# Kernel optimization log

Measured on AMD Instinct MI355X. Metric: run time of the kernel, lower is better.

## Reference

```python
import jax, jax.numpy as jnp
import numpy as np

LN_EPS = 1e-5   # torch LayerNorm default
EPS = 1e-8      # slot-attention renorm eps
ITERS = 3


def _ln(x, g, b):
    m = jnp.mean(x, axis=-1, keepdims=True)
    v = jnp.mean(jnp.square(x - m), axis=-1, keepdims=True)
    return (x - m) * jax.lax.rsqrt(v + LN_EPS) * g + b


def _gru(x, h, W_ih, W_hh, b_ih, b_hh):
    # torch GRUCell: gates ordered r, z, n; weight_* has shape [3h, in]
    gi = x @ W_ih.T + b_ih
    gh = h @ W_hh.T + b_hh
    ir, iz, inn = jnp.split(gi, 3, axis=-1)
    hr, hz, hn = jnp.split(gh, 3, axis=-1)
    r = jax.nn.sigmoid(ir + hr)
    z = jax.nn.sigmoid(iz + hz)
    n = jnp.tanh(inn + r * hn)
    return (1.0 - z) * n + z * h


def setup_inputs() -> dict:
    key = jax.random.key(0)
    ks = jax.random.split(key, 16)
    b, n, d, n_s = 32, 4096, 256, 8
    h = max(d, 128)  # hidden_dim = max(dim, hidden_dim)
    s = 1.0 / np.sqrt(d)
    inp = {
        "inputs": jax.random.normal(ks[0], (b, n, d), jnp.float32),
        "noise": jax.random.normal(ks[1], (b, n_s, d), jnp.float32),
        "slots_mu": jax.random.normal(ks[2], (1, 1, d), jnp.float32),
        "slots_logsigma": jax.random.normal(ks[3], (1, 1, d), jnp.float32) * 0.1,
        "Wq": jax.random.uniform(ks[4], (d, d), jnp.float32, -s, s),
        "bq": jnp.zeros((d,), jnp.float32),
        "Wk": jax.random.uniform(ks[5], (d, d), jnp.float32, -s, s),
        "bk": jnp.zeros((d,), jnp.float32),
        "Wv": jax.random.uniform(ks[6], (d, d), jnp.float32, -s, s),
        "bv": jnp.zeros((d,), jnp.float32),
        "W_ih": jax.random.uniform(ks[7], (3 * d, d), jnp.float32, -s, s),
        "W_hh": jax.random.uniform(ks[8], (3 * d, d), jnp.float32, -s, s),
        "b_ih": jnp.zeros((3 * d,), jnp.float32),
        "b_hh": jnp.zeros((3 * d,), jnp.float32),
        "W1": jax.random.uniform(ks[9], (h, d), jnp.float32, -s, s),
        "b1": jnp.zeros((h,), jnp.float32),
        "W2": jax.random.uniform(ks[10], (d, h), jnp.float32, -s, s),
        "b2": jnp.zeros((d,), jnp.float32),
        "g_in": jnp.ones((d,), jnp.float32), "be_in": jnp.zeros((d,), jnp.float32),
        "g_sl": jnp.ones((d,), jnp.float32), "be_sl": jnp.zeros((d,), jnp.float32),
        "g_ff": jnp.ones((d,), jnp.float32), "be_ff": jnp.zeros((d,), jnp.float32),
    }
    return inp


def reference(inputs, noise, slots_mu, slots_logsigma, Wq, bq, Wk, bk, Wv, bv,
              W_ih, W_hh, b_ih, b_hh, W1, b1, W2, b2,
              g_in, be_in, g_sl, be_sl, g_ff, be_ff):
    b, n, d = inputs.shape
    scale = d ** (-0.5)
    # reparameterized slot init
    slots = slots_mu + jnp.exp(slots_logsigma) * noise          # [b, n_s, d]
    x = _ln(inputs, g_in, be_in)
    k = x @ Wk.T + bk                                           # [b, n, d]
    v = x @ Wv.T + bv
    attn = None
    for _ in range(ITERS):
        slots_prev = slots
        q = _ln(slots, g_sl, be_sl) @ Wq.T + bq                 # [b, n_s, d]
        dots = jnp.einsum('bid,bjd->bij', q, k) * scale         # [b, n_s, n]
        attn = jax.nn.softmax(dots, axis=1)                     # softmax over SLOTS
        attn_ = attn + EPS
        attn_ = attn_ / jnp.sum(attn_, axis=-1, keepdims=True)  # renorm over inputs
        updates = jnp.einsum('bjd,bij->bid', v, attn_)          # [b, n_s, d]
        slots = _gru(updates.reshape(-1, d), slots_prev.reshape(-1, d),
                     W_ih, W_hh, b_ih, b_hh).reshape(b, -1, d)
        pre = _ln(slots, g_ff, be_ff)
        slots = slots + (jax.nn.relu(pre @ W1.T + b1) @ W2.T + b2)
    return (slots, attn)
```

## Files before the change

kernel.cpp:

```cpp
#include <hip/hip_runtime.h>
#include <hip/hip_fp16.h>
#include <cstdint>
#include <cstddef>


#define NTOK 4096
#define DDIM 256
#define NSLOT 8
#define NBATCH 32
#define NCHK 64
#define SROWS (NBATCH * NSLOT)
#define SCALE 0.0625f
#define LN_EPS_C 1e-5f
#define ATTN_EPS_C 1e-8f

__device__ __forceinline__ void wave_reduce2(float& s, float& ss) {
#pragma unroll
  for (int off = 32; off > 0; off >>= 1) {
    s  += __shfl_down(s, off, 64);
    ss += __shfl_down(ss, off, 64);
  }
}
__device__ __forceinline__ void wave_reduce3(float& a, float& b, float& c) {
#pragma unroll
  for (int off = 32; off > 0; off >>= 1) {
    a += __shfl_down(a, off, 64);
    b += __shfl_down(b, off, 64);
    c += __shfl_down(c, off, 64);
  }
}

__global__ __launch_bounds__(256) void transpose_all_k(
    const float* __restrict__ Wq, const float* __restrict__ Wv,
    const float* __restrict__ Wih, const float* __restrict__ Whh,
    const float* __restrict__ W1, const float* __restrict__ W2,
    float* __restrict__ WqT, float* __restrict__ WvT,
    float* __restrict__ WihT, float* __restrict__ WhhT,
    float* __restrict__ W1T, float* __restrict__ W2T) {
  __shared__ float tile[32][33];
  int bz = blockIdx.x;
  const float* in; float* out; int O, bo;
  if (bz < 8)       { in = Wq;  out = WqT;  O = 256; bo = bz; }
  else if (bz < 16) { in = Wv;  out = WvT;  O = 256; bo = bz - 8; }
  else if (bz < 40) { in = Wih; out = WihT; O = 768; bo = bz - 16; }
  else if (bz < 64) { in = Whh; out = WhhT; O = 768; bo = bz - 40; }
  else if (bz < 72) { in = W1;  out = W1T;  O = 256; bo = bz - 64; }
  else              { in = W2;  out = W2T;  O = 256; bo = bz - 72; }
  int tx = threadIdx.x & 31, ty = threadIdx.x >> 5;
  int ro = bo * 32, cd = blockIdx.y * 32;
#pragma unroll
  for (int p = 0; p < 32; p += 8)
    tile[ty + p][tx] = in[(size_t)(ro + ty + p) * DDIM + cd + tx];
  __syncthreads();
#pragma unroll
  for (int p = 0; p < 32; p += 8)
    out[(size_t)(cd + ty + p) * O + ro + tx] = tile[tx][ty + p];
}

__device__ __forceinline__ void qk_tail(
    float newslot, int r, int t, const float* __restrict__ g_sl,
    const float* __restrict__ be_sl, const float* __restrict__ WqT,
    const float* __restrict__ bq, const float* __restrict__ Wk,
    const float* __restrict__ bk, const float* __restrict__ g_in,
    const float* __restrict__ be_in, float* __restrict__ qk,
    float* __restrict__ C0, float* __restrict__ G, float* ln, float* sq,
    float* red) {
  float s = newslot, ss = newslot * newslot;
  wave_reduce2(s, ss);
  int lane = t & 63, wid = t >> 6;
  if (lane == 0) { red[wid] = s; red[4 + wid] = ss; }
  __syncthreads();
  s = red[0] + red[1] + red[2] + red[3];
  ss = red[4] + red[5] + red[6] + red[7];
  float m = s * (1.f / DDIM);
  float rs = rsqrtf(ss * (1.f / DDIM) - m * m + LN_EPS_C);
  ln[t] = (newslot - m) * rs * g_sl[t] + be_sl[t];
  __syncthreads();
  float q = bq[t];
  {
    const float* p = WqT + t;
#pragma unroll 8
    for (int d = 0; d < DDIM; ++d) q = fmaf(ln[d], p[(size_t)d * DDIM], q);
  }
  sq[t] = q;
  __syncthreads();
  float a2 = 0.f;
  {
    const float* p = Wk + t;
#pragma unroll 8
    for (int o = 0; o < DDIM; ++o) a2 = fmaf(sq[o], p[(size_t)o * DDIM], a2);
  }
  float qkv = SCALE * a2;
  qk[(size_t)r * DDIM + t] = qkv;
  float v0 = q * bk[t], v1 = g_in[t] * qkv, v2 = be_in[t] * qkv;
  wave_reduce3(v0, v1, v2);
  __syncthreads();
  if (lane == 0) { red[wid] = v0; red[4 + wid] = v1; red[8 + wid] = v2; }
  __syncthreads();
  if (t == 0) {
    float qkb = SCALE * (red[0] + red[1] + red[2] + red[3]);
    float Gv = red[4] + red[5] + red[6] + red[7];
    float Bv = red[8] + red[9] + red[10] + red[11];
    C0[r] = qkb + Bv;
    G[r] = Gv;
  }
}

__global__ __launch_bounds__(256) void init_q_qk_k(
    const float* __restrict__ noise, const float* __restrict__ mu,
    const float* __restrict__ logsig, float* __restrict__ slots,
    const float* __restrict__ g_sl, const float* __restrict__ be_sl,
    const float* __restrict__ WqT, const float* __restrict__ bq,
    const float* __restrict__ Wk, const float* __restrict__ bk,
    const float* __restrict__ g_in, const float* __restrict__ be_in,
    float* __restrict__ qk, float* __restrict__ C0, float* __restrict__ G) {
  __shared__ float ln[DDIM], sq[DDIM], red[12];
  int r = blockIdx.x, t = threadIdx.x;
  float ns = mu[t] + expf(logsig[t]) * noise[(size_t)r * DDIM + t];
  slots[(size_t)r * DDIM + t] = ns;
  qk_tail(ns, r, t, g_sl, be_sl, WqT, bq, Wk, bk, g_in, be_in, qk, C0, G, ln,
          sq, red);
}

__global__ __launch_bounds__(256) void fused_attn_k(
    const float* __restrict__ X, const float* __restrict__ g,
    const float* __restrict__ be, const float* __restrict__ qk,
    const float* __restrict__ C0, const float* __restrict__ Gv,
    float* __restrict__ attn_out, float* __restrict__ S_part,
    __half* __restrict__ u_part, int write_attn) {
  __shared__ float sx[32][260];
  __shared__ float sqkg[NSLOT][DDIM];
  __shared__ float part[8][10][32];
  __shared__ float sm[32], srd[32];
  __shared__ float sC0[NSLOT], sG[NSLOT], sS[NSLOT];
  int b = blockIdx.x, c = blockIdx.y, t = threadIdx.x;
  int tj = t & 31, qd = t >> 5;
#pragma unroll
  for (int i = 0; i < NSLOT; ++i)
    sqkg[i][t] = qk[((size_t)b * NSLOT + i) * DDIM + t] * g[t];
  if (t < NSLOT) { sC0[t] = C0[b * NSLOT + t]; sG[t] = Gv[b * NSLOT + t]; sS[t] = 0.f; }
  float gt = g[t], bet = be[t];
  float acc[NSLOT] = {};
  const size_t base = (size_t)b * NTOK + (size_t)c * 64;
#pragma unroll
  for (int half = 0; half < 2; ++half) {
    __syncthreads();
#pragma unroll
    for (int it = 0; it < 8; ++it) {
      int e = it * 256 + t;
      int row = e >> 6, c4 = e & 63;
      float4 v = *(const float4*)(X + (base + half * 32 + row) * DDIM + c4 * 4);
      *(float4*)&sx[row][c4 * 4] = v;
    }
    __syncthreads();
    float s = 0.f, ss = 0.f, p[NSLOT] = {};
#pragma unroll
    for (int d4 = 0; d4 < 8; ++d4) {
      float4 xv = *(const float4*)&sx[tj][qd * 32 + d4 * 4];
      s += xv.x + xv.y + xv.z + xv.w;
      ss += xv.x * xv.x + xv.y * xv.y + xv.z * xv.z + xv.w * xv.w;
#pragma unroll
      for (int i = 0; i < NSLOT; ++i) {
        float4 qv = *(const float4*)&sqkg[i][qd * 32 + d4 * 4];
        p[i] += xv.x * qv.x + xv.y * qv.y + xv.z * qv.z + xv.w * qv.w;
      }
    }
#pragma unroll
    for (int i = 0; i < NSLOT; ++i) part[qd][i][tj] = p[i];
    part[qd][8][tj] = s;
    part[qd][9][tj] = ss;
    __syncthreads();
    if (t < 32) {
      float s1 = 0.f, s2 = 0.f;
#pragma unroll
      for (int q2 = 0; q2 < 8; ++q2) { s1 += part[q2][8][t]; s2 += part[q2][9][t]; }
      float m = s1 * (1.f / DDIM);
      float rs = rsqrtf(s2 * (1.f / DDIM) - m * m + LN_EPS_C);
      sm[t] = m;
      srd[t] = rs;
      float dots[NSLOT], mx = -1e30f;
#pragma unroll
      for (int i = 0; i < NSLOT; ++i) {
        float P1 = 0.f;
#pragma unroll
        for (int q2 = 0; q2 < 8; ++q2) P1 += part[q2][i][t];
        dots[i] = rs * (P1 - m * sG[i]) + sC0[i];
        mx = fmaxf(mx, dots[i]);
      }
      float sum = 0.f;
#pragma unroll
      for (int i = 0; i < NSLOT; ++i) { dots[i] = expf(dots[i] - mx); sum += dots[i]; }
      float inv = 1.f / sum;
#pragma unroll
      for (int i = 0; i < NSLOT; ++i) {
        float a = dots[i] * inv;
        if (write_attn)
          attn_out[((size_t)b * NSLOT + i) * NTOK + c * 64 + half * 32 + t] = a;
        float ae = a + ATTN_EPS_C;
        part[i][8][t] = ae;
        float ps = ae;
#pragma unroll
        for (int off = 16; off > 0; off >>= 1) ps += __shfl_down(ps, off, 64);
        if (t == 0) sS[i] += ps;
      }
    }
    __syncthreads();
#pragma unroll 8
    for (int jj = 0; jj < 32; ++jj) {
      float x = sx[jj][t];
      float xl = (x - sm[jj]) * srd[jj] * gt + bet;
#pragma unroll
      for (int i = 0; i < NSLOT; ++i) acc[i] = fmaf(xl, part[i][8][jj], acc[i]);
    }
  }
  __half* upb = u_part + (((size_t)b * NCHK + c) * NSLOT) * DDIM + t;
#pragma unroll
  for (int i = 0; i < NSLOT; ++i) upb[(size_t)i * DDIM] = __float2half(acc[i]);
  if (t < NSLOT) S_part[((size_t)b * NCHK + c) * NSLOT + t] = sS[t];
}

__global__ __launch_bounds__(1024) void slot_update_k(
    const __half* __restrict__ u_part, const float* __restrict__ S_part,
    const float* __restrict__ slots_in, const float* __restrict__ WvT,
    const float* __restrict__ bv, const float* __restrict__ WihT,
    const float* __restrict__ WhhT, const float* __restrict__ b_ih,
    const float* __restrict__ b_hh, const float* __restrict__ g_ff,
    const float* __restrict__ be_ff, const float* __restrict__ W1T,
    const float* __restrict__ b1, const float* __restrict__ W2T,
    const float* __restrict__ b2, const float* __restrict__ g_sl,
    const float* __restrict__ be_sl, const float* __restrict__ WqT,
    const float* __restrict__ bq, const float* __restrict__ Wk,
    const float* __restrict__ bk, const float* __restrict__ g_in,
    const float* __restrict__ be_in, float* __restrict__ slots_out,
    float* __restrict__ qk, float* __restrict__ C0, float* __restrict__ G,
    int compute_qk) {
  __shared__ float red[4][6][DDIM];
  __shared__ float su[DDIM], sh[DDIM], supd[DDIM], v1[DDIM], v2[DDIM];
  __shared__ float scal[16];
  int r = blockIdx.x, t = threadIdx.x;
  int b = r >> 3, i = r & 7;
  int o = t & 255, ks = t >> 8;
  int lane = t & 63, wid = t >> 6;
  {
    float up = 0.f;
    const __half* upp =
        u_part + (((size_t)b * NCHK + ks * 16) * NSLOT + i) * DDIM + o;
#pragma unroll
    for (int cc = 0; cc < 16; ++cc)
      up += __half2float(upp[(size_t)cc * (NSLOT * DDIM)]);
    red[ks][0][o] = up;
  }
  if (t < 64) {
    float sp = S_part[((size_t)b * NCHK + t) * NSLOT + i];
#pragma unroll
    for (int off = 32; off > 0; off >>= 1) sp += __shfl_down(sp, off, 64);
    if (t == 0) scal[0] = sp;
  }
  if (ks == 0) sh[o] = slots_in[(size_t)r * DDIM + o];
  __syncthreads();
  if (ks == 0) {
    float invS = 1.f / scal[0];
    su[o] = (red[0][0][o] + red[1][0][o] + red[2][0][o] + red[3][0][o]) * invS;
  }
  __syncthreads();
  {
    float p = 0.f;
    const float* wp = WvT + (size_t)(ks * 64) * DDIM + o;
#pragma unroll 8
    for (int dd = 0; dd < 64; ++dd)
      p = fmaf(su[ks * 64 + dd], wp[(size_t)dd * DDIM], p);
    red[ks][0][o] = p;
  }
  __syncthreads();
  if (ks == 0)
    supd[o] = bv[o] + red[0][0][o] + red[1][0][o] + red[2][0][o] + red[3][0][o];
  __syncthreads();
  {
    float p0 = 0, p1 = 0, p2 = 0, p3 = 0, p4 = 0, p5 = 0;
    const float* pi = WihT + (size_t)(ks * 64) * (3 * DDIM) + o;
    const float* ph = WhhT + (size_t)(ks * 64) * (3 * DDIM) + o;
#pragma unroll 4
    for (int dd = 0; dd < 64; ++dd) {
      float ud = supd[ks * 64 + dd], hd = sh[ks * 64 + dd];
      size_t off = (size_t)dd * (3 * DDIM);
      p0 = fmaf(ud, pi[off], p0);
      p1 = fmaf(ud, pi[off + DDIM], p1);
      p2 = fmaf(ud, pi[off + 2 * DDIM], p2);
      p3 = fmaf(hd, ph[off], p3);
      p4 = fmaf(hd, ph[off + DDIM], p4);
      p5 = fmaf(hd, ph[off + 2 * DDIM], p5);
    }
    red[ks][0][o] = p0; red[ks][1][o] = p1; red[ks][2][o] = p2;
    red[ks][3][o] = p3; red[ks][4][o] = p4; red[ks][5][o] = p5;
  }
  __syncthreads();
  if (ks == 0) {
    float air = b_ih[o] + red[0][0][o] + red[1][0][o] + red[2][0][o] + red[3][0][o];
    float aiz = b_ih[DDIM + o] + red[0][1][o] + red[1][1][o] + red[2][1][o] + red[3][1][o];
    float ain = b_ih[2 * DDIM + o] + red[0][2][o] + red[1][2][o] + red[2][2][o] + red[3][2][o];
    float ahr = b_hh[o] + red[0][3][o] + red[1][3][o] + red[2][3][o] + red[3][3][o];
    float ahz = b_hh[DDIM + o] + red[0][4][o] + red[1][4][o] + red[2][4][o] + red[3][4][o];
    float ahn = b_hh[2 * DDIM + o] + red[0][5][o] + red[1][5][o] + red[2][5][o] + red[3][5][o];
    float rg = 1.f / (1.f + expf(-(air + ahr)));
    float zg = 1.f / (1.f + expf(-(aiz + ahz)));
    float ng = tanhf(ain + rg * ahn);
    float nh = (1.f - zg) * ng + zg * sh[o];
    v1[o] = nh;
    float s2 = nh, ss2 = nh * nh;
    wave_reduce2(s2, ss2);
    if (lane == 0) { scal[wid] = s2; scal[4 + wid] = ss2; }
  }
  __syncthreads();
  if (ks == 0) {
    float sS = scal[0] + scal[1] + scal[2] + scal[3];
    float sQ = scal[4] + scal[5] + scal[6] + scal[7];
    float m = sS * (1.f / DDIM);
    float rs = rsqrtf(sQ * (1.f / DDIM) - m * m + LN_EPS_C);
    v2[o] = (v1[o] - m) * rs * g_ff[o] + be_ff[o];
  }
  __syncthreads();
  {
    float p = 0.f;
    const float* wp = W1T + (size_t)(ks * 64) * DDIM + o;
#pragma unroll 8
    for (int dd = 0; dd < 64; ++dd)
      p = fmaf(v2[ks * 64 + dd], wp[(size_t)dd * DDIM], p);
    red[ks][0][o] = p;
  }
  __syncthreads();
  if (ks == 0)
    su[o] = fmaxf(b1[o] + red[0][0][o] + red[1][0][o] + red[2][0][o] + red[3][0][o], 0.f);
  __syncthreads();
  {
    float p = 0.f;
    const float* wp = W2T + (size_t)(ks * 64) * DDIM + o;
#pragma unroll 8
    for (int dd = 0; dd < 64; ++dd)
      p = fmaf(su[ks * 64 + dd], wp[(size_t)dd * DDIM], p);
    red[ks][0][o] = p;
  }
  __syncthreads();
  if (ks == 0) {
    float out = v1[o] + b2[o] + red[0][0][o] + red[1][0][o] + red[2][0][o] + red[3][0][o];
    slots_out[(size_t)r * DDIM + o] = out;
    v2[o] = out;
  }
  __syncthreads();
  if (!compute_qk) return;
  if (ks == 0) {
    float x = v2[o];
    float s2 = x, ss2 = x * x;
    wave_reduce2(s2, ss2);
    if (lane == 0) { scal[wid] = s2; scal[4 + wid] = ss2; }
  }
  __syncthreads();
  if (ks == 0) {
    float sS = scal[0] + scal[1] + scal[2] + scal[3];
    float sQ = scal[4] + scal[5] + scal[6] + scal[7];
    float m = sS * (1.f / DDIM);
    float rs = rsqrtf(sQ * (1.f / DDIM) - m * m + LN_EPS_C);
    su[o] = (v2[o] - m) * rs * g_sl[o] + be_sl[o];
  }
  __syncthreads();
  {
    float p = 0.f;
    const float* wp = WqT + (size_t)(ks * 64) * DDIM + o;
#pragma unroll 8
    for (int dd = 0; dd < 64; ++dd)
      p = fmaf(su[ks * 64 + dd], wp[(size_t)dd * DDIM], p);
    red[ks][0][o] = p;
  }
  __syncthreads();
  if (ks == 0)
    sh[o] = bq[o] + red[0][0][o] + red[1][0][o] + red[2][0][o] + red[3][0][o];
  __syncthreads();
  {
    float p = 0.f;
    const float* wp = Wk + (size_t)(ks * 64) * DDIM + o;
#pragma unroll 8
    for (int dd = 0; dd < 64; ++dd)
      p = fmaf(sh[ks * 64 + dd], wp[(size_t)dd * DDIM], p);
    red[ks][0][o] = p;
  }
  __syncthreads();
  if (ks == 0) {
    float qkv = SCALE * (red[0][0][o] + red[1][0][o] + red[2][0][o] + red[3][0][o]);
    qk[(size_t)r * DDIM + o] = qkv;
    float v0 = sh[o] * bk[o], vG = g_in[o] * qkv, vB = be_in[o] * qkv;
    wave_reduce3(v0, vG, vB);
    if (lane == 0) { scal[wid] = v0; scal[4 + wid] = vG; scal[8 + wid] = vB; }
  }
  __syncthreads();
  if (t == 0) {
    float qkb = SCALE * (scal[0] + scal[1] + scal[2] + scal[3]);
    G[r] = scal[4] + scal[5] + scal[6] + scal[7];
    C0[r] = qkb + scal[8] + scal[9] + scal[10] + scal[11];
  }
}

extern "C" void kernel_launch(void* const* d_in, const int* in_sizes, int n_in,
                              void* d_out, int out_size, void* d_ws,
                              size_t ws_size, hipStream_t stream) {
  const float* inputs   = (const float*)d_in[0];
  const float* noise    = (const float*)d_in[1];
  const float* slots_mu = (const float*)d_in[2];
  const float* slots_ls = (const float*)d_in[3];
  const float* Wq   = (const float*)d_in[4];
  const float* bq   = (const float*)d_in[5];
  const float* Wk   = (const float*)d_in[6];
  const float* bk   = (const float*)d_in[7];
  const float* Wv   = (const float*)d_in[8];
  const float* bv   = (const float*)d_in[9];
  const float* W_ih = (const float*)d_in[10];
  const float* W_hh = (const float*)d_in[11];
  const float* b_ih = (const float*)d_in[12];
  const float* b_hh = (const float*)d_in[13];
  const float* W1   = (const float*)d_in[14];
  const float* b1   = (const float*)d_in[15];
  const float* W2   = (const float*)d_in[16];
  const float* b2   = (const float*)d_in[17];
  const float* g_in = (const float*)d_in[18];
  const float* be_in= (const float*)d_in[19];
  const float* g_sl = (const float*)d_in[20];
  const float* be_sl= (const float*)d_in[21];
  const float* g_ff = (const float*)d_in[22];
  const float* be_ff= (const float*)d_in[23];

  float* out_slots = (float*)d_out;
  float* out_attn  = (float*)d_out + SROWS * DDIM;

  float* w = (float*)d_ws;
  float* slots = w;  w += SROWS * DDIM;
  float* qk = w;     w += SROWS * DDIM;
  float* C0 = w;     w += SROWS;
  float* G = w;      w += SROWS;
  float* WqT = w;    w += DDIM * DDIM;
  float* WvT = w;    w += DDIM * DDIM;
  float* WihT = w;   w += DDIM * 3 * DDIM;
  float* WhhT = w;   w += DDIM * 3 * DDIM;
  float* W1T = w;    w += DDIM * DDIM;
  float* W2T = w;    w += DDIM * DDIM;
  float* S_part = w; w += NBATCH * NCHK * NSLOT;
  __half* u_part = (__half*)w;

  transpose_all_k<<<dim3(80, 8), 256, 0, stream>>>(
      Wq, Wv, W_ih, W_hh, W1, W2, WqT, WvT, WihT, WhhT, W1T, W2T);
  init_q_qk_k<<<SROWS, 256, 0, stream>>>(noise, slots_mu, slots_ls, slots,
                                         g_sl, be_sl, WqT, bq, Wk, bk, g_in,
                                         be_in, qk, C0, G);
  for (int it = 0; it < 3; ++it) {
    fused_attn_k<<<dim3(NBATCH, NCHK), 256, 0, stream>>>(
        inputs, g_in, be_in, qk, C0, G, out_attn, S_part, u_part,
        (it == 2) ? 1 : 0);
    float* sout = (it == 2) ? out_slots : slots;
    slot_update_k<<<SROWS, 1024, 0, stream>>>(
        u_part, S_part, slots, WvT, bv, WihT, WhhT, b_ih, b_hh, g_ff, be_ff,
        W1T, b1, W2T, b2, g_sl, be_sl, WqT, bq, Wk, bk, g_in, be_in, sout, qk,
        C0, G, (it == 2) ? 0 : 1);
  }
}
```

Baseline: 284.2 us.

## Cache LayerNormed inputs as fp16 and store weights in half precision

The first attention pass normalizes the fp32 inputs and writes them as an fp16 buffer. Later iterations read that buffer with a simpler fp16 attention kernel that no longer recomputes LayerNorm statistics. All transposed weight matrices, plus Wk, are converted to fp16 to halve weight traffic in the slot update, and the slot-init/q kernel is folded into slot_update_k. This cuts repeated fp32 reads of the large input tensor at the cost of an extra 64MB write and reduced precision.

```diff
diff --git a/kernel.cpp b/kernel.cpp
--- a/kernel.cpp
+++ b/kernel.cpp
@@ -30,23 +30,32 @@
   }
 }
 
-__global__ __launch_bounds__(256) void transpose_all_k(
+__global__ __launch_bounds__(256) void convert_weights_k(
     const float* __restrict__ Wq, const float* __restrict__ Wv,
     const float* __restrict__ Wih, const float* __restrict__ Whh,
     const float* __restrict__ W1, const float* __restrict__ W2,
-    float* __restrict__ WqT, float* __restrict__ WvT,
-    float* __restrict__ WihT, float* __restrict__ WhhT,
-    float* __restrict__ W1T, float* __restrict__ W2T) {
+    const float* __restrict__ Wk, __half* __restrict__ WqT,
+    __half* __restrict__ WvT, __half* __restrict__ WihT,
+    __half* __restrict__ WhhT, __half* __restrict__ W1T,
+    __half* __restrict__ W2T, __half* __restrict__ Wk_h) {
   __shared__ float tile[32][33];
   int bz = blockIdx.x;
-  const float* in; float* out; int O, bo;
+  int tx = threadIdx.x & 31, ty = threadIdx.x >> 5;
+  if (bz >= 80) {
+    int ro = (bz - 80) * 32, cd = blockIdx.y * 32;
+#pragma unroll
+    for (int p = 0; p < 32; p += 8)
+      Wk_h[(size_t)(ro + ty + p) * DDIM + cd + tx] =
+          __float2half(Wk[(size_t)(ro + ty + p) * DDIM + cd + tx]);
+    return;
+  }
+  const float* in; __half* out; int O, bo;
   if (bz < 8)       { in = Wq;  out = WqT;  O = 256; bo = bz; }
   else if (bz < 16) { in = Wv;  out = WvT;  O = 256; bo = bz - 8; }
   else if (bz < 40) { in = Wih; out = WihT; O = 768; bo = bz - 16; }
   else if (bz < 64) { in = Whh; out = WhhT; O = 768; bo = bz - 40; }
   else if (bz < 72) { in = W1;  out = W1T;  O = 256; bo = bz - 64; }
   else              { in = W2;  out = W2T;  O = 256; bo = bz - 72; }
-  int tx = threadIdx.x & 31, ty = threadIdx.x >> 5;
   int ro = bo * 32, cd = blockIdx.y * 32;
 #pragma unroll
   for (int p = 0; p < 32; p += 8)
@@ -54,80 +63,15 @@
   __syncthreads();
 #pragma unroll
   for (int p = 0; p < 32; p += 8)
-    out[(size_t)(cd + ty + p) * O + ro + tx] = tile[tx][ty + p];
-}
-
-__device__ __forceinline__ void qk_tail(
-    float newslot, int r, int t, const float* __restrict__ g_sl,
-    const float* __restrict__ be_sl, const float* __restrict__ WqT,
-    const float* __restrict__ bq, const float* __restrict__ Wk,
-    const float* __restrict__ bk, const float* __restrict__ g_in,
-    const float* __restrict__ be_in, float* __restrict__ qk,
-    float* __restrict__ C0, float* __restrict__ G, float* ln, float* sq,
-    float* red) {
-  float s = newslot, ss = newslot * newslot;
-  wave_reduce2(s, ss);
-  int lane = t & 63, wid = t >> 6;
-  if (lane == 0) { red[wid] = s; red[4 + wid] = ss; }
-  __syncthreads();
-  s = red[0] + red[1] + red[2] + red[3];
-  ss = red[4] + red[5] + red[6] + red[7];
-  float m = s * (1.f / DDIM);
-  float rs = rsqrtf(ss * (1.f / DDIM) - m * m + LN_EPS_C);
-  ln[t] = (newslot - m) * rs * g_sl[t] + be_sl[t];
-  __syncthreads();
-  float q = bq[t];
-  {
-    const float* p = WqT + t;
-#pragma unroll 8
-    for (int d = 0; d < DDIM; ++d) q = fmaf(ln[d], p[(size_t)d * DDIM], q);
-  }
-  sq[t] = q;
-  __syncthreads();
-  float a2 = 0.f;
-  {
-    const float* p = Wk + t;
-#pragma unroll 8
-    for (int o = 0; o < DDIM; ++o) a2 = fmaf(sq[o], p[(size_t)o * DDIM], a2);
-  }
-  float qkv = SCALE * a2;
-  qk[(size_t)r * DDIM + t] = qkv;
-  float v0 = q * bk[t], v1 = g_in[t] * qkv, v2 = be_in[t] * qkv;
-  wave_reduce3(v0, v1, v2);
-  __syncthreads();
-  if (lane == 0) { red[wid] = v0; red[4 + wid] = v1; red[8 + wid] = v2; }
-  __syncthreads();
-  if (t == 0) {
-    float qkb = SCALE * (red[0] + red[1] + red[2] + red[3]);
-    float Gv = red[4] + red[5] + red[6] + red[7];
-    float Bv = red[8] + red[9] + red[10] + red[11];
-    C0[r] = qkb + Bv;
-    G[r] = Gv;
-  }
-}
-
-__global__ __launch_bounds__(256) void init_q_qk_k(
-    const float* __restrict__ noise, const float* __restrict__ mu,
-    const float* __restrict__ logsig, float* __restrict__ slots,
-    const float* __restrict__ g_sl, const float* __restrict__ be_sl,
-    const float* __restrict__ WqT, const float* __restrict__ bq,
-    const float* __restrict__ Wk, const float* __restrict__ bk,
-    const float* __restrict__ g_in, const float* __restrict__ be_in,
-    float* __restrict__ qk, float* __restrict__ C0, float* __restrict__ G) {
-  __shared__ float ln[DDIM], sq[DDIM], red[12];
-  int r = blockIdx.x, t = threadIdx.x;
-  float ns = mu[t] + expf(logsig[t]) * noise[(size_t)r * DDIM + t];
-  slots[(size_t)r * DDIM + t] = ns;
-  qk_tail(ns, r, t, g_sl, be_sl, WqT, bq, Wk, bk, g_in, be_in, qk, C0, G, ln,
-          sq, red);
-}
-
-__global__ __launch_bounds__(256) void fused_attn_k(
+    out[(size_t)(cd + ty + p) * O + ro + tx] = __float2half(tile[tx][ty + p]);
+}
+
+__global__ __launch_bounds__(256) void fused_attn_f32_k(
     const float* __restrict__ X, const float* __restrict__ g,
     const float* __restrict__ be, const float* __restrict__ qk,
     const float* __restrict__ C0, const float* __restrict__ Gv,
-    float* __restrict__ attn_out, float* __restrict__ S_part,
-    __half* __restrict__ u_part, int write_attn) {
+    float* __restrict__ S_part, __half* __restrict__ u_part,
+    __half* __restrict__ xh_out) {
   __shared__ float sx[32][260];
   __shared__ float sqkg[NSLOT][DDIM];
   __shared__ float part[8][10][32];
@@ -193,10 +137,7 @@
       float inv = 1.f / sum;
 #pragma unroll
       for (int i = 0; i < NSLOT; ++i) {
-        float a = dots[i] * inv;
-        if (write_attn)
-          attn_out[((size_t)b * NSLOT + i) * NTOK + c * 64 + half * 32 + t] = a;
-        float ae = a + ATTN_EPS_C;
+        float ae = dots[i] * inv + ATTN_EPS_C;
         part[i][8][t] = ae;
         float ps = ae;
 #pragma unroll
@@ -209,6 +150,7 @@
     for (int jj = 0; jj < 32; ++jj) {
       float x = sx[jj][t];
       float xl = (x - sm[jj]) * srd[jj] * gt + bet;
+      xh_out[(base + half * 32 + jj) * DDIM + t] = __float2half(xl);
 #pragma unroll
       for (int i = 0; i < NSLOT; ++i) acc[i] = fmaf(xl, part[i][8][jj], acc[i]);
     }
@@ -219,21 +161,111 @@
   if (t < NSLOT) S_part[((size_t)b * NCHK + c) * NSLOT + t] = sS[t];
 }
 
+__global__ __launch_bounds__(256) void fused_attn_f16_k(
+    const __half* __restrict__ xh, const float* __restrict__ qk,
+    const float* __restrict__ qkb, float* __restrict__ attn_out,
+    float* __restrict__ S_part, __half* __restrict__ u_part, int write_attn) {
+  __shared__ __half sx[64][258];
+  __shared__ float2 sqkf[NSLOT][128];
+  __shared__ float part[4][NSLOT][64];
+  __shared__ float sa[NSLOT][64];
+  __shared__ float sC0[NSLOT], sS[NSLOT];
+  int b = blockIdx.x, c = blockIdx.y, t = threadIdx.x;
+  {
+    int i = t >> 5, p2 = t & 31;
+    const float* qr = qk + ((size_t)b * NSLOT + i) * DDIM;
+#pragma unroll
+    for (int kk = 0; kk < 4; ++kk) {
+      int col = p2 * 4 + kk;
+      sqkf[i][col] = make_float2(qr[col * 2], qr[col * 2 + 1]);
+    }
+  }
+  if (t < NSLOT) sC0[t] = qkb[b * NSLOT + t];
+  const size_t base = (size_t)b * NTOK + (size_t)c * 64;
+#pragma unroll
+  for (int it = 0; it < 8; ++it) {
+    int e = it * 256 + t;
+    int row = e >> 5, c8 = e & 31;
+    const __half* src = xh + (base + row) * DDIM + c8 * 8;
+    uint4 v = *(const uint4*)src;
+    __half2* dst = (__half2*)&sx[row][c8 * 8];
+    dst[0] = ((const __half2*)&v)[0];
+    dst[1] = ((const __half2*)&v)[1];
+    dst[2] = ((const __half2*)&v)[2];
+    dst[3] = ((const __half2*)&v)[3];
+  }
+  __syncthreads();
+  int tj = t & 63, qd = t >> 6;
+  float p[NSLOT] = {};
+  const __half2* xrow = (const __half2*)&sx[tj][qd * 64];
+#pragma unroll
+  for (int dd2 = 0; dd2 < 32; ++dd2) {
+    float2 xf = __half22float2(xrow[dd2]);
+#pragma unroll
+    for (int i = 0; i < NSLOT; ++i) {
+      float2 qf = sqkf[i][qd * 32 + dd2];
+      p[i] = fmaf(xf.x, qf.x, fmaf(xf.y, qf.y, p[i]));
+    }
+  }
+#pragma unroll
+  for (int i = 0; i < NSLOT; ++i) part[qd][i][tj] = p[i];
+  __syncthreads();
+  if (t < 64) {
+    float dots[NSLOT], mx = -1e30f;
+#pragma unroll
+    for (int i = 0; i < NSLOT; ++i) {
+      dots[i] = part[0][i][t] + part[1][i][t] + part[2][i][t] + part[3][i][t] +
+                sC0[i];
+      mx = fmaxf(mx, dots[i]);
+    }
+    float sum = 0.f;
+#pragma unroll
+    for (int i = 0; i < NSLOT; ++i) { dots[i] = expf(dots[i] - mx); sum += dots[i]; }
+    float inv = 1.f / sum;
+#pragma unroll
+    for (int i = 0; i < NSLOT; ++i) {
+      float a = dots[i] * inv;
+      if (write_attn)
+        attn_out[((size_t)b * NSLOT + i) * NTOK + c * 64 + t] = a;
+      float ae = a + ATTN_EPS_C;
+      sa[i][t] = ae;
+      float ps = ae;
+#pragma unroll
+      for (int off = 32; off > 0; off >>= 1) ps += __shfl_down(ps, off, 64);
+      if (t == 0) sS[i] = ps;
+    }
+  }
+  __syncthreads();
+  float acc[NSLOT] = {};
+#pragma unroll 8
+  for (int jj = 0; jj < 64; ++jj) {
+    float x = __half2float(sx[jj][t]);
+#pragma unroll
+    for (int i = 0; i < NSLOT; ++i) acc[i] = fmaf(x, sa[i][jj], acc[i]);
+  }
+  __half* upb = u_part + (((size_t)b * NCHK + c) * NSLOT) * DDIM + t;
+#pragma unroll
+  for (int i = 0; i < NSLOT; ++i) upb[(size_t)i * DDIM] = __float2half(acc[i]);
+  if (t < NSLOT) S_part[((size_t)b * NCHK + c) * NSLOT + t] = sS[t];
+}
+
 __global__ __launch_bounds__(1024) void slot_update_k(
     const __half* __restrict__ u_part, const float* __restrict__ S_part,
-    const float* __restrict__ slots_in, const float* __restrict__ WvT,
-    const float* __restrict__ bv, const float* __restrict__ WihT,
-    const float* __restrict__ WhhT, const float* __restrict__ b_ih,
+    const float* __restrict__ slots_in, const __half* __restrict__ WvT,
+    const float* __restrict__ bv, const __half* __restrict__ WihT,
+    const __half* __restrict__ WhhT, const float* __restrict__ b_ih,
     const float* __restrict__ b_hh, const float* __restrict__ g_ff,
-    const float* __restrict__ be_ff, const float* __restrict__ W1T,
-    const float* __restrict__ b1, const float* __restrict__ W2T,
+    const float* __restrict__ be_ff, const __half* __restrict__ W1T,
+    const float* __restrict__ b1, const __half* __restrict__ W2T,
     const float* __restrict__ b2, const float* __restrict__ g_sl,
-    const float* __restrict__ be_sl, const float* __restrict__ WqT,
-    const float* __restrict__ bq, const float* __restrict__ Wk,
+    const float* __restrict__ be_sl, const __half* __restrict__ WqT,
+    const float* __restrict__ bq, const __half* __restrict__ Wk_h,
     const float* __restrict__ bk, const float* __restrict__ g_in,
-    const float* __restrict__ be_in, float* __restrict__ slots_out,
-    float* __restrict__ qk, float* __restrict__ C0, float* __restrict__ G,
-    int compute_qk) {
+    const float* __restrict__ be_in, const float* __restrict__ noise,
+    const float* __restrict__ mu, const float* __restrict__ logsig,
+    float* __restrict__ slots_out, float* __restrict__ qk,
+    float* __restrict__ C0, float* __restrict__ qkb_out,
+    float* __restrict__ G, int init, int compute_qk) {
   __shared__ float red[4][6][DDIM];
   __shared__ float su[DDIM], sh[DDIM], supd[DDIM], v1[DDIM], v2[DDIM];
   __shared__ float scal[16];
@@ -241,111 +273,120 @@
   int b = r >> 3, i = r & 7;
   int o = t & 255, ks = t >> 8;
   int lane = t & 63, wid = t >> 6;
-  {
-    float up = 0.f;
-    const __half* upp =
-        u_part + (((size_t)b * NCHK + ks * 16) * NSLOT + i) * DDIM + o;
-#pragma unroll
-    for (int cc = 0; cc < 16; ++cc)
-      up += __half2float(upp[(size_t)cc * (NSLOT * DDIM)]);
-    red[ks][0][o] = up;
-  }
-  if (t < 64) {
-    float sp = S_part[((size_t)b * NCHK + t) * NSLOT + i];
-#pragma unroll
-    for (int off = 32; off > 0; off >>= 1) sp += __shfl_down(sp, off, 64);
-    if (t == 0) scal[0] = sp;
-  }
-  if (ks == 0) sh[o] = slots_in[(size_t)r * DDIM + o];
-  __syncthreads();
-  if (ks == 0) {
-    float invS = 1.f / scal[0];
-    su[o] = (red[0][0][o] + red[1][0][o] + red[2][0][o] + red[3][0][o]) * invS;
-  }
-  __syncthreads();
-  {
-    float p = 0.f;
-    const float* wp = WvT + (size_t)(ks * 64) * DDIM + o;
-#pragma unroll 8
-    for (int dd = 0; dd < 64; ++dd)
-      p = fmaf(su[ks * 64 + dd], wp[(size_t)dd * DDIM], p);
-    red[ks][0][o] = p;
-  }
-  __syncthreads();
-  if (ks == 0)
-    supd[o] = bv[o] + red[0][0][o] + red[1][0][o] + red[2][0][o] + red[3][0][o];
-  __syncthreads();
-  {
-    float p0 = 0, p1 = 0, p2 = 0, p3 = 0, p4 = 0, p5 = 0;
-    const float* pi = WihT + (size_t)(ks * 64) * (3 * DDIM) + o;
-    const float* ph = WhhT + (size_t)(ks * 64) * (3 * DDIM) + o;
+  if (init) {
+    if (ks == 0) {
+      float ns = mu[o] + expf(logsig[o]) * noise[(size_t)r * DDIM + o];
+      slots_out[(size_t)r * DDIM + o] = ns;
+      v2[o] = ns;
+    }
+    __syncthreads();
+  } else {
+    {
+      float up = 0.f;
+      const __half* upp =
+          u_part + (((size_t)b * NCHK + ks * 16) * NSLOT + i) * DDIM + o;
+#pragma unroll
+      for (int cc = 0; cc < 16; ++cc)
+        up += __half2float(upp[(size_t)cc * (NSLOT * DDIM)]);
+      red[ks][0][o] = up;
+    }
+    if (t < 64) {
+      float sp = S_part[((size_t)b * NCHK + t) * NSLOT + i];
+#pragma unroll
+      for (int off = 32; off > 0; off >>= 1) sp += __shfl_down(sp, off, 64);
+      if (t == 0) scal[0] = sp;
+    }
+    if (ks == 0) sh[o] = slots_in[(size_t)r * DDIM + o];
+    __syncthreads();
+    if (ks == 0) {
+      float invS = 1.f / scal[0];
+      su[o] = (red[0][0][o] + red[1][0][o] + red[2][0][o] + red[3][0][o]) * invS;
+    }
+    __syncthreads();
+    {
+      float p = 0.f;
+      const __half* wp = WvT + (size_t)(ks * 64) * DDIM + o;
+#pragma unroll 8
+      for (int dd = 0; dd < 64; ++dd)
+        p = fmaf(su[ks * 64 + dd], __half2float(wp[(size_t)dd * DDIM]), p);
+      red[ks][0][o] = p;
+    }
+    __syncthreads();
+    if (ks == 0)
+      supd[o] = bv[o] + red[0][0][o] + red[1][0][o] + red[2][0][o] + red[3][0][o];
+    __syncthreads();
+    {
+      float p0 = 0, p1 = 0, p2 = 0, p3 = 0, p4 = 0, p5 = 0;
+      const __half* pi = WihT + (size_t)(ks * 64) * (3 * DDIM) + o;
+      const __half* ph = WhhT + (size_t)(ks * 64) * (3 * DDIM) + o;
 #pragma unroll 4
-    for (int dd = 0; dd < 64; ++dd) {
-      float ud = supd[ks * 64 + dd], hd = sh[ks * 64 + dd];
-      size_t off = (size_t)dd * (3 * DDIM);
-      p0 = fmaf(ud, pi[off], p0);
-      p1 = fmaf(ud, pi[off + DDIM], p1);
-      p2 = fmaf(ud, pi[off + 2 * DDIM], p2);
-      p3 = fmaf(hd, ph[off], p3);
-      p4 = fmaf(hd, ph[off + DDIM], p4);
-      p5 = fmaf(hd, ph[off + 2 * DDIM], p5);
-    }
-    red[ks][0][o] = p0; red[ks][1][o] = p1; red[ks][2][o] = p2;
-    red[ks][3][o] = p3; red[ks][4][o] = p4; red[ks][5][o] = p5;
-  }
-  __syncthreads();
-  if (ks == 0) {
-    float air = b_ih[o] + red[0][0][o] + red[1][0][o] + red[2][0][o] + red[3][0][o];
-    float aiz = b_ih[DDIM + o] + red[0][1][o] + red[1][1][o] + red[2][1][o] + red[3][1][o];
-    float ain = b_ih[2 * DDIM + o] + red[0][2][o] + red[1][2][o] + red[2][2][o] + red[3][2][o];
-    float ahr = b_hh[o] + red[0][3][o] + red[1][3][o] + red[2][3][o] + red[3][3][o];
-    float ahz = b_hh[DDIM + o] + red[0][4][o] + red[1][4][o] + red[2][4][o] + red[3][4][o];
-    float ahn = b_hh[2 * DDIM + o] + red[0][5][o] + red[1][5][o] + red[2][5][o] + red[3][5][o];
-    float rg = 1.f / (1.f + expf(-(air + ahr)));
-    float zg = 1.f / (1.f + expf(-(aiz + ahz)));
-    float ng = tanhf(ain + rg * ahn);
-    float nh = (1.f - zg) * ng + zg * sh[o];
-    v1[o] = nh;
-    float s2 = nh, ss2 = nh * nh;
-    wave_reduce2(s2, ss2);
-    if (lane == 0) { scal[wid] = s2; scal[4 + wid] = ss2; }
-  }
-  __syncthreads();
-  if (ks == 0) {
-    float sS = scal[0] + scal[1] + scal[2] + scal[3];
-    float sQ = scal[4] + scal[5] + scal[6] + scal[7];
-    float m = sS * (1.f / DDIM);
-    float rs = rsqrtf(sQ * (1.f / DDIM) - m * m + LN_EPS_C);
-    v2[o] = (v1[o] - m) * rs * g_ff[o] + be_ff[o];
-  }
-  __syncthreads();
-  {
-    float p = 0.f;
-    const float* wp = W1T + (size_t)(ks * 64) * DDIM + o;
-#pragma unroll 8
-    for (int dd = 0; dd < 64; ++dd)
-      p = fmaf(v2[ks * 64 + dd], wp[(size_t)dd * DDIM], p);
-    red[ks][0][o] = p;
-  }
-  __syncthreads();
-  if (ks == 0)
-    su[o] = fmaxf(b1[o] + red[0][0][o] + red[1][0][o] + red[2][0][o] + red[3][0][o], 0.f);
-  __syncthreads();
-  {
-    float p = 0.f;
-    const float* wp = W2T + (size_t)(ks * 64) * DDIM + o;
-#pragma unroll 8
-    for (int dd = 0; dd < 64; ++dd)
-      p = fmaf(su[ks * 64 + dd], wp[(size_t)dd * DDIM], p);
-    red[ks][0][o] = p;
-  }
-  __syncthreads();
-  if (ks == 0) {
-    float out = v1[o] + b2[o] + red[0][0][o] + red[1][0][o] + red[2][0][o] + red[3][0][o];
-    slots_out[(size_t)r * DDIM + o] = out;
-    v2[o] = out;
-  }
-  __syncthreads();
+      for (int dd = 0; dd < 64; ++dd) {
+        float ud = supd[ks * 64 + dd], hd = sh[ks * 64 + dd];
+        size_t off = (size_t)dd * (3 * DDIM);
+        p0 = fmaf(ud, __half2float(pi[off]), p0);
+        p1 = fmaf(ud, __half2float(pi[off + DDIM]), p1);
+        p2 = fmaf(ud, __half2float(pi[off + 2 * DDIM]), p2);
+        p3 = fmaf(hd, __half2float(ph[off]), p3);
+        p4 = fmaf(hd, __half2float(ph[off + DDIM]), p4);
+        p5 = fmaf(hd, __half2float(ph[off + 2 * DDIM]), p5);
+      }
+      red[ks][0][o] = p0; red[ks][1][o] = p1; red[ks][2][o] = p2;
+      red[ks][3][o] = p3; red[ks][4][o] = p4; red[ks][5][o] = p5;
+    }
+    __syncthreads();
+    if (ks == 0) {
+      float air = b_ih[o] + red[0][0][o] + red[1][0][o] + red[2][0][o] + red[3][0][o];
+      float aiz = b_ih[DDIM + o] + red[0][1][o] + red[1][1][o] + red[2][1][o] + red[3][1][o];
+      float ain = b_ih[2 * DDIM + o] + red[0][2][o] + red[1][2][o] + red[2][2][o] + red[3][2][o];
+      float ahr = b_hh[o] + red[0][3][o] + red[1][3][o] + red[2][3][o] + red[3][3][o];
+      float ahz = b_hh[DDIM + o] + red[0][4][o] + red[1][4][o] + red[2][4][o] + red[3][4][o];
+      float ahn = b_hh[2 * DDIM + o] + red[0][5][o] + red[1][5][o] + red[2][5][o] + red[3][5][o];
+      float rg = 1.f / (1.f + expf(-(air + ahr)));
+      float zg = 1.f / (1.f + expf(-(aiz + ahz)));
+      float ng = tanhf(ain + rg * ahn);
+      float nh = (1.f - zg) * ng + zg * sh[o];
+      v1[o] = nh;
+      float s2 = nh, ss2 = nh * nh;
+      wave_reduce2(s2, ss2);
+      if (lane == 0) { scal[wid] = s2; scal[4 + wid] = ss2; }
+    }
+    __syncthreads();
+    if (ks == 0) {
+      float sS = scal[0] + scal[1] + scal[2] + scal[3];
+      float sQ = scal[4] + scal[5] + scal[6] + scal[7];
+      float m = sS * (1.f / DDIM);
+      float rs = rsqrtf(sQ * (1.f / DDIM) - m * m + LN_EPS_C);
+      v2[o] = (v1[o] - m) * rs * g_ff[o] + be_ff[o];
+    }
+    __syncthreads();
+    {
+      float p = 0.f;
+      const __half* wp = W1T + (size_t)(ks * 64) * DDIM + o;
+#pragma unroll 8
+      for (int dd = 0; dd < 64; ++dd)
+        p = fmaf(v2[ks * 64 + dd], __half2float(wp[(size_t)dd * DDIM]), p);
+      red[ks][0][o] = p;
+    }
+    __syncthreads();
+    if (ks == 0)
+      su[o] = fmaxf(b1[o] + red[0][0][o] + red[1][0][o] + red[2][0][o] + red[3][0][o], 0.f);
+    __syncthreads();
+    {
+      float p = 0.f;
+      const __half* wp = W2T + (size_t)(ks * 64) * DDIM + o;
+#pragma unroll 8
+      for (int dd = 0; dd < 64; ++dd)
+        p = fmaf(su[ks * 64 + dd], __half2float(wp[(size_t)dd * DDIM]), p);
+      red[ks][0][o] = p;
+    }
+    __syncthreads();
+    if (ks == 0) {
+      float out = v1[o] + b2[o] + red[0][0][o] + red[1][0][o] + red[2][0][o] + red[3][0][o];
+      slots_out[(size_t)r * DDIM + o] = out;
+      v2[o] = out;
+    }
+    __syncthreads();
+  }
   if (!compute_qk) return;
   if (ks == 0) {
     float x = v2[o];
@@ -364,10 +405,10 @@
   __syncthreads();
   {
     float p = 0.f;
-    const float* wp = WqT + (size_t)(ks * 64) * DDIM + o;
+    const __half* wp = WqT + (size_t)(ks * 64) * DDIM + o;
 #pragma unroll 8
     for (int dd = 0; dd < 64; ++dd)
-      p = fmaf(su[ks * 64 + dd], wp[(size_t)dd * DDIM], p);
+      p = fmaf(su[ks * 64 + dd], __half2float(wp[(size_t)dd * DDIM]), p);
     red[ks][0][o] = p;
   }
   __syncthreads();
@@ -376,10 +417,10 @@
   __syncthreads();
   {
     float p = 0.f;
-    const float* wp = Wk + (size_t)(ks * 64) * DDIM + o;
+    const __half* wp = Wk_h + (size_t)(ks * 64) * DDIM + o;
 #pragma unroll 8
     for (int dd = 0; dd < 64; ++dd)
-      p = fmaf(sh[ks * 64 + dd], wp[(size_t)dd * DDIM], p);
+      p = fmaf(sh[ks * 64 + dd], __half2float(wp[(size_t)dd * DDIM]), p);
     red[ks][0][o] = p;
   }
   __syncthreads();
@@ -393,6 +434,7 @@
   __syncthreads();
   if (t == 0) {
     float qkb = SCALE * (scal[0] + scal[1] + scal[2] + scal[3]);
+    qkb_out[r] = qkb;
     G[r] = scal[4] + scal[5] + scal[6] + scal[7];
     C0[r] = qkb + scal[8] + scal[9] + scal[10] + scal[11];
   }
@@ -433,29 +475,43 @@
   float* slots = w;  w += SROWS * DDIM;
   float* qk = w;     w += SROWS * DDIM;
   float* C0 = w;     w += SROWS;
+  float* qkb = w;    w += SROWS;
   float* G = w;      w += SROWS;
-  float* WqT = w;    w += DDIM * DDIM;
-  float* WvT = w;    w += DDIM * DDIM;
-  float* WihT = w;   w += DDIM * 3 * DDIM;
-  float* WhhT = w;   w += DDIM * 3 * DDIM;
-  float* W1T = w;    w += DDIM * DDIM;
-  float* W2T = w;    w += DDIM * DDIM;
   float* S_part = w; w += NBATCH * NCHK * NSLOT;
-  __half* u_part = (__half*)w;
-
-  transpose_all_k<<<dim3(80, 8), 256, 0, stream>>>(
-      Wq, Wv, W_ih, W_hh, W1, W2, WqT, WvT, WihT, WhhT, W1T, W2T);
-  init_q_qk_k<<<SROWS, 256, 0, stream>>>(noise, slots_mu, slots_ls, slots,
-                                         g_sl, be_sl, WqT, bq, Wk, bk, g_in,
-                                         be_in, qk, C0, G);
-  for (int it = 0; it < 3; ++it) {
-    fused_attn_k<<<dim3(NBATCH, NCHK), 256, 0, stream>>>(
-        inputs, g_in, be_in, qk, C0, G, out_attn, S_part, u_part,
-        (it == 2) ? 1 : 0);
-    float* sout = (it == 2) ? out_slots : slots;
-    slot_update_k<<<SROWS, 1024, 0, stream>>>(
-        u_part, S_part, slots, WvT, bv, WihT, WhhT, b_ih, b_hh, g_ff, be_ff,
-        W1T, b1, W2T, b2, g_sl, be_sl, WqT, bq, Wk, bk, g_in, be_in, sout, qk,
-        C0, G, (it == 2) ? 0 : 1);
-  }
-}
+  __half* h = (__half*)w;
+  __half* xh = h;     h += (size_t)NBATCH * NTOK * DDIM;
+  __half* u_part = h; h += (size_t)NBATCH * NCHK * NSLOT * DDIM;
+  __half* WqT_h = h;  h += DDIM * DDIM;
+  __half* WvT_h = h;  h += DDIM * DDIM;
+  __half* WihT_h = h; h += DDIM * 3 * DDIM;
+  __half* WhhT_h = h; h += DDIM * 3 * DDIM;
+  __half* W1T_h = h;  h += DDIM * DDIM;
+  __half* W2T_h = h;  h += DDIM * DDIM;
+  __half* Wk_h = h;   h += DDIM * DDIM;
+
+  convert_weights_k<<<dim3(88, 8), 256, 0, stream>>>(
+      Wq, Wv, W_ih, W_hh, W1, W2, Wk, WqT_h, WvT_h, WihT_h, WhhT_h, W1T_h,
+      W2T_h, Wk_h);
+  slot_update_k<<<SROWS, 1024, 0, stream>>>(
+      u_part, S_part, slots, WvT_h, bv, WihT_h, WhhT_h, b_ih, b_hh, g_ff,
+      be_ff, W1T_h, b1, W2T_h, b2, g_sl, be_sl, WqT_h, bq, Wk_h, bk, g_in,
+      be_in, noise, slots_mu, slots_ls, slots, qk, C0, qkb, G, 1, 1);
+  fused_attn_f32_k<<<dim3(NBATCH, NCHK), 256, 0, stream>>>(
+      inputs, g_in, be_in, qk, C0, G, S_part, u_part, xh);
+  slot_update_k<<<SROWS, 1024, 0, stream>>>(
+      u_part, S_part, slots, WvT_h, bv, WihT_h, WhhT_h, b_ih, b_hh, g_ff,
+      be_ff, W1T_h, b1, W2T_h, b2, g_sl, be_sl, WqT_h, bq, Wk_h, bk, g_in,
+      be_in, noise, slots_mu, slots_ls, slots, qk, C0, qkb, G, 0, 1);
+  fused_attn_f16_k<<<dim3(NBATCH, NCHK), 256, 0, stream>>>(
+      xh, qk, qkb, out_attn, S_part, u_part, 0);
+  slot_update_k<<<SROWS, 1024, 0, stream>>>(
+      u_part, S_part, slots, WvT_h, bv, WihT_h, WhhT_h, b_ih, b_hh, g_ff,
+      be_ff, W1T_h, b1, W2T_h, b2, g_sl, be_sl, WqT_h, bq, Wk_h, bk, g_in,
+      be_in, noise, slots_mu, slots_ls, slots, qk, C0, qkb, G, 0, 1);
+  fused_attn_f16_k<<<dim3(NBATCH, NCHK), 256, 0, stream>>>(
+      xh, qk, qkb, out_attn, S_part, u_part, 1);
+  slot_update_k<<<SROWS, 1024, 0, stream>>>(
+      u_part, S_part, slots, WvT_h, bv, WihT_h, WhhT_h, b_ih, b_hh, g_ff,
+      be_ff, W1T_h, b1, W2T_h, b2, g_sl, be_sl, WqT_h, bq, Wk_h, bk, g_in,
+      be_in, noise, slots_mu, slots_ls, out_slots, qk, C0, qkb, G, 0, 0);
+}
```

After: 236.8 us. -16.7%, faster.
